# Kernel optimization log

Measured on AMD Instinct MI355X. Metric: run time of the kernel, lower is better.

The kernel has to match this reference:

```python
import jax, jax.numpy as jnp
import numpy as np

NH = 4       # n_heads
R = 3        # n_rounds
LN_EPS = 1e-5
NEG = -1e9   # large negative for masked attention (avoids NaN on fully-masked rows)


def _mha(q, k, v, w, b, block=None):
    # w: [4, D, D] = (Wq, Wk, Wv, Wo); b: [4, D]. batch_first MHA, no dropout (eval).
    B, Nq, Dm = q.shape
    hd = Dm // NH

    def proj(x, wi, bi):
        return (x @ wi + bi).reshape(B, -1, NH, hd).transpose(0, 2, 1, 3)  # [B,h,N,hd]

    Q = proj(q, w[0], b[0])
    K = proj(k, w[1], b[1])
    V = proj(v, w[2], b[2])
    s = jnp.einsum('bhqd,bhkd->bhqk', Q, K) * (1.0 / np.sqrt(hd))
    if block is not None:  # block[b,q,k]=True means masked out
        s = jnp.where(block[:, None, :, :], NEG, s)
    p = jax.nn.softmax(s, axis=-1)
    o = jnp.einsum('bhqk,bhkd->bhqd', p, V).transpose(0, 2, 1, 3).reshape(B, -1, Dm)
    return o @ w[3] + b[3]


def setup_inputs() -> dict:
    key = jax.random.key(0)
    ks = jax.random.split(key, 16)
    B, N, Dm = 256, 128, 256
    s = 0.02
    return {
        'H': jax.random.normal(ks[0], (B, N, Dm), jnp.float32),
        'pred_heads': jax.random.randint(ks[1], (B, N), 0, N),
        'mask': jnp.ones((B, N), jnp.float32),
        'ha_w': jax.random.normal(ks[2], (R, 4, Dm, Dm)) * s,
        'ha_b': jnp.zeros((R, 4, Dm)),
        'sa_w': jax.random.normal(ks[3], (R, 4, Dm, Dm)) * s,
        'sa_b': jnp.zeros((R, 4, Dm)),
        'ct_w': jax.random.normal(ks[4], (R, 2 * Dm, Dm)) * s,
        'ct_b': jnp.zeros((R, Dm)),
        'gate_w': jax.random.normal(ks[5], (R, 4 * Dm, Dm)) * s,
        'gate_b': jnp.zeros((R, Dm)),
        'tr_w': jax.random.normal(ks[6], (R, 4 * Dm, Dm)) * s,
        'tr_b': jnp.zeros((R, Dm)),
        'ln_g': jnp.ones((R, Dm)),
        'ln_b': jnp.zeros((R, Dm)),
        'arc_head_w': jax.random.normal(ks[7], (Dm, Dm)) * s,
        'arc_head_b': jnp.zeros((Dm,)),
        'arc_dep_w': jax.random.normal(ks[8], (Dm, Dm)) * s,
        'arc_dep_b': jnp.zeros((Dm,)),
        'bilinear': jax.random.normal(ks[9], (Dm, Dm)) * np.sqrt(2.0 / Dm).astype(np.float32),
        'bh_w': jax.random.normal(ks[10], (Dm,)) * s,
        'bh_b': jnp.zeros(()),
        'bd_w': jax.random.normal(ks[11], (Dm,)) * s,
        'bd_b': jnp.zeros(()),
    }


def reference(H, pred_heads, mask, ha_w, ha_b, sa_w, sa_b, ct_w, ct_b,
              gate_w, gate_b, tr_w, tr_b, ln_g, ln_b,
              arc_head_w, arc_head_b, arc_dep_w, arc_dep_b, bilinear,
              bh_w, bh_b, bd_w, bd_b):
    B, N, Dm = H.shape
    mb = mask > 0
    hi = jnp.clip(pred_heads, 0, N - 1)
    hi3 = jnp.broadcast_to(hi[:, :, None], (B, N, Dm))
    bidx = jnp.arange(B)[:, None]
    eye = jnp.eye(N, dtype=bool)
    # sibling mask: same predicted head, not self, both positions valid (constant across rounds)
    sib = (pred_heads[:, :, None] == pred_heads[:, None, :]) & ~eye[None] \
          & mb[:, None, :] & mb[:, :, None]
    block = ~sib

    Hr = H
    for i in range(R):
        # gather head representation, attend to it
        head_repr = jnp.take_along_axis(Hr, hi3, axis=1)
        head_msg = _mha(Hr, head_repr, head_repr, ha_w[i], ha_b[i])
        # scatter-add children onto their heads, average
        child_sum = jnp.zeros_like(Hr).at[bidx, hi].add(Hr)
        child_count = jnp.zeros((B, N), Hr.dtype).at[bidx, hi].add(mask)
        child_avg = child_sum / jnp.maximum(child_count, 1.0)[:, :, None]
        child_msg = jax.nn.gelu(
            jnp.concatenate([Hr, child_avg], -1) @ ct_w[i] + ct_b[i], approximate=False)
        # masked sibling self-attention (N <= 128 branch)
        sib_msg = _mha(Hr, Hr, Hr, sa_w[i], sa_b[i], block=block)
        # gated fuse + residual + LayerNorm
        comb = jnp.concatenate([Hr, head_msg, child_msg, sib_msg], -1)
        g = jax.nn.sigmoid(comb @ gate_w[i] + gate_b[i])
        u = jax.nn.gelu(comb @ tr_w[i] + tr_b[i], approximate=False)
        Hn = Hr + g * u
        mu = Hn.mean(-1, keepdims=True)
        var = ((Hn - mu) ** 2).mean(-1, keepdims=True)
        Hr = (Hn - mu) / jnp.sqrt(var + LN_EPS) * ln_g[i] + ln_b[i]

    h_head = Hr @ arc_head_w + arc_head_b
    h_dep = Hr @ arc_dep_w + arc_dep_b
    scores = jnp.einsum('bnd,de,bme->bnm', h_head, bilinear, h_dep)
    scores = scores + (h_head @ bh_w + bh_b)[:, None, :] + (h_dep @ bd_w + bd_b)[:, :, None]
    return Hr, scores
```

## Files before the change

### kernel.cpp

```cpp
#include <hip/hip_runtime.h>
#include <hip/hip_bf16.h>
#include <math.h>

typedef __hip_bfloat16 bf16;
typedef __attribute__((ext_vector_type(8))) short bf16x8v;
typedef __attribute__((ext_vector_type(4))) float f32x4v;

#define BD 256
#define NN 128
#define DM 256
#define NHD 4
#define HDIM 64
#define RR 3

__device__ __forceinline__ float b2f(bf16 x) { return __bfloat162float(x); }
__device__ __forceinline__ bf16 f2b(float x) { return __float2bfloat16(x); }
__device__ __forceinline__ float geluf(float x) { return 0.5f * x * (1.f + erff(x * 0.70710678118654752f)); }

#define GLOAD16(g, l) __builtin_amdgcn_global_load_lds( \
    (const __attribute__((address_space(1))) void*)(g), \
    (__attribute__((address_space(3))) void*)(l), 16, 0, 0)

__global__ __launch_bounds__(256) void cvt32to16_kernel(
    const float* __restrict__ in, bf16* __restrict__ out, int n)
{
  int i = blockIdx.x * 256 + threadIdx.x;
  int stride = gridDim.x * 256;
  for (; i < n; i += stride) out[i] = f2b(in[i]);
}

__global__ __launch_bounds__(256) void cvt16to32_kernel(
    const bf16* __restrict__ in, float* __restrict__ out, int n)
{
  int i = blockIdx.x * 256 + threadIdx.x;
  int stride = gridDim.x * 256;
  for (; i < n; i += stride) out[i] = b2f(in[i]);
}

struct TDesc { const float* src; bf16* dst; int K; int base; };
struct TTable { TDesc e[11]; };

__global__ __launch_bounds__(256) void transpose_w_kernel(TTable T, int nent)
{
  int t = blockIdx.x;
  int ei = 0;
  for (int i = 1; i < nent; i++) if (t >= T.e[i].base) ei = i;
  const float* src = T.e[ei].src;
  bf16* dst = T.e[ei].dst;
  int K = T.e[ei].K;
  int lt = t - T.e[ei].base;
  int nt = lt & 7, kt = lt >> 3;

  __shared__ float tile[32][33];
  int tx = threadIdx.x & 31, ty = threadIdx.x >> 5;
#pragma unroll
  for (int i = 0; i < 4; i++)
    tile[ty + i * 8][tx] = src[(size_t)(kt * 32 + ty + i * 8) * 256 + nt * 32 + tx];
  __syncthreads();
#pragma unroll
  for (int i = 0; i < 4; i++)
    dst[(size_t)(nt * 32 + ty + i * 8) * K + kt * 32 + tx] = f2b(tile[tx][ty + i * 8]);
}

struct GJob {
  const bf16 *a0, *a1, *a2, *a3;
  const int* gather;
  const bf16* Wt;
  const float* bias;
  bf16* out;
  int K, act, transp;
};
struct GJobs8 { GJob j[8]; };

__global__ __launch_bounds__(256) void gemm_multi_kernel(GJobs8 J)
{
  const GJob jb = J.j[blockIdx.y];
  const int b  = blockIdx.x & 255;
  const int nh = blockIdx.x >> 8;
  const int tid = threadIdx.x;
  const int w = tid >> 6;
  const int lane = tid & 63;
  const int wr = w >> 1, wc = w & 1;
  const int r16 = lane & 15;
  const int kg = lane >> 4;
  const int K = jb.K;
  const int nk = K >> 5;
  const int c0 = nh * 128;

  __shared__ __align__(16) char lds[32768];

  const int srow = tid >> 2;
  const int skc  = tid & 3;
  int g0 = srow, g1 = srow + 64;
  if (jb.gather) {
    int t0 = jb.gather[b * NN + srow];      g0 = min(max(t0, 0), NN - 1);
    int t1 = jb.gather[b * NN + srow + 64]; g1 = min(max(t1, 0), NN - 1);
  }
  const size_t aoff0 = ((size_t)b * NN + g0) * DM + skc * 8;
  const size_t aoff1 = ((size_t)b * NN + g1) * DM + skc * 8;
  const bf16* wsrc0 = jb.Wt + (size_t)(c0 + srow) * K + skc * 8;
  const bf16* wsrc1 = jb.Wt + (size_t)(c0 + srow + 64) * K + skc * 8;
  const int wbase = w * 1024;

  f32x4v zero = {0.f, 0.f, 0.f, 0.f};
  f32x4v acc[4][4];
#pragma unroll
  for (int mi = 0; mi < 4; mi++)
#pragma unroll
    for (int ni = 0; ni < 4; ni++) acc[mi][ni] = zero;

  int a_ro[4], w_ro[4];
#pragma unroll
  for (int mi = 0; mi < 4; mi++)
    a_ro[mi] = (wr * 64 + mi * 16 + r16) * 64 + kg * 16;
#pragma unroll
  for (int ni = 0; ni < 4; ni++)
    w_ro[ni] = (wc * 64 + ni * 16 + r16) * 64 + kg * 16;

  {
    const bf16* Ab = jb.a0;
    GLOAD16(Ab + aoff0, lds + wbase);
    GLOAD16(Ab + aoff1, lds + 4096 + wbase);
    GLOAD16(wsrc0,      lds + 16384 + wbase);
    GLOAD16(wsrc1,      lds + 16384 + 4096 + wbase);
  }
  __syncthreads();

  int cur = 0;
  for (int kt = 0; kt < nk; kt++) {
    if (kt + 1 < nk) {
      int k0 = (kt + 1) << 5;
      int sg = k0 >> 8;
      const bf16* Ab = (sg == 0) ? jb.a0 : ((sg == 1) ? jb.a1 : ((sg == 2) ? jb.a2 : jb.a3));
      int ko = k0 & 255;
      int nb = (cur ^ 1) * 8192;
      GLOAD16(Ab + aoff0 + ko,  lds + nb + wbase);
      GLOAD16(Ab + aoff1 + ko,  lds + nb + 4096 + wbase);
      GLOAD16(wsrc0 + k0,       lds + 16384 + nb + wbase);
      GLOAD16(wsrc1 + k0,       lds + 16384 + nb + 4096 + wbase);
    }

    const char* La = lds + cur * 8192;
    const char* Lw = lds + 16384 + cur * 8192;
    bf16x8v a[4], ww[4];
#pragma unroll
    for (int mi = 0; mi < 4; mi++) a[mi] = *(const bf16x8v*)(La + a_ro[mi]);
#pragma unroll
    for (int ni = 0; ni < 4; ni++) ww[ni] = *(const bf16x8v*)(Lw + w_ro[ni]);
#pragma unroll
    for (int mi = 0; mi < 4; mi++)
#pragma unroll
      for (int ni = 0; ni < 4; ni++)
        acc[mi][ni] = __builtin_amdgcn_mfma_f32_16x16x32_bf16(a[mi], ww[ni], acc[mi][ni], 0, 0, 0);

    __syncthreads();
    cur ^= 1;
  }

#pragma unroll
  for (int ni = 0; ni < 4; ni++) {
    int col = c0 + wc * 64 + ni * 16 + r16;
    float bv = jb.bias ? jb.bias[col] : 0.f;
#pragma unroll
    for (int mi = 0; mi < 4; mi++) {
      int row0 = wr * 64 + mi * 16 + kg * 4;
      if (!jb.transp) {
        size_t base = ((size_t)b * NN + row0) * DM + col;
#pragma unroll
        for (int r = 0; r < 4; r++) {
          float x = acc[mi][ni][r] + bv;
          if (jb.act == 1) x = geluf(x);
          jb.out[base + (size_t)r * DM] = f2b(x);
        }
      } else {
        size_t base = ((size_t)b * DM + col) * NN + row0;
#pragma unroll
        for (int r = 0; r < 4; r++) {
          float x = acc[mi][ni][r] + bv;
          if (jb.act == 1) x = geluf(x);
          jb.out[base + r] = f2b(x);
        }
      }
    }
  }
}

struct AttnArgs {
  const bf16 *Qa, *Ka, *Va; bf16* Oa;
  const bf16 *Qs, *Ks, *Vs; bf16* Os;
};

__global__ __launch_bounds__(256) void attn2_kernel(
    AttnArgs A, const int* __restrict__ ph, const float* __restrict__ mask)
{
  const int b = blockIdx.y, h = blockIdx.x;
  const bool has_mask = (blockIdx.z == 1);
  const bf16* Qb = has_mask ? A.Qs : A.Qa;
  const bf16* Kb = has_mask ? A.Ks : A.Ka;
  const bf16* Vt = has_mask ? A.Vs : A.Va;
  bf16* Ob       = has_mask ? A.Os : A.Oa;

  const int w = threadIdx.x >> 6;
  const int lane = threadIdx.x & 63;
  const int r16 = lane & 15, kg = lane >> 4;
  const int q0 = w * 32;

  __shared__ bf16 P_lds[4][32 * 128];
  __shared__ int   ph_sh[NN];
  __shared__ float mk_sh[NN];

  if (has_mask && threadIdx.x < NN) {
    ph_sh[threadIdx.x] = ph[(size_t)b * NN + threadIdx.x];
    mk_sh[threadIdx.x] = mask[(size_t)b * NN + threadIdx.x];
  }
  __syncthreads();

  const bf16* Qh = Qb + (size_t)b * NN * DM + (size_t)h * HDIM;
  const bf16* Kh = Kb + (size_t)b * NN * DM + (size_t)h * HDIM;
  const bf16* Vh = Vt + ((size_t)b * DM + (size_t)h * HDIM) * NN;

  f32x4v zero = {0.f, 0.f, 0.f, 0.f};

  f32x4v accs[2][8];
#pragma unroll
  for (int mi = 0; mi < 2; mi++)
#pragma unroll
    for (int ni = 0; ni < 8; ni++) accs[mi][ni] = zero;

#pragma unroll
  for (int ks = 0; ks < 2; ks++) {
    int d = ks * 32 + kg * 8;
    bf16x8v a[2], bb[8];
#pragma unroll
    for (int mi = 0; mi < 2; mi++)
      a[mi] = *(const bf16x8v*)(Qh + (size_t)(q0 + mi * 16 + r16) * DM + d);
#pragma unroll
    for (int ni = 0; ni < 8; ni++)
      bb[ni] = *(const bf16x8v*)(Kh + (size_t)(ni * 16 + r16) * DM + d);
#pragma unroll
    for (int mi = 0; mi < 2; mi++)
#pragma unroll
      for (int ni = 0; ni < 8; ni++)
        accs[mi][ni] = __builtin_amdgcn_mfma_f32_16x16x32_bf16(a[mi], bb[ni], accs[mi][ni], 0, 0, 0);
  }

#pragma unroll
  for (int mi = 0; mi < 2; mi++) {
#pragma unroll
    for (int r = 0; r < 4; r++) {
      int wq = mi * 16 + kg * 4 + r;
      int q_e = q0 + wq;
      float v[8];
      float mx = -3.0e38f;
      int qp = 0; float qm = 1.f;
      if (has_mask) { qp = ph_sh[q_e]; qm = mk_sh[q_e]; }
#pragma unroll
      for (int ni = 0; ni < 8; ni++) {
        float s = accs[mi][ni][r] * 0.125f;
        if (has_mask) {
          int t_e = ni * 16 + r16;
          bool sib = (qp == ph_sh[t_e]) && (q_e != t_e) && (qm > 0.f) && (mk_sh[t_e] > 0.f);
          if (!sib) s = -1e9f;
        }
        v[ni] = s;
        mx = fmaxf(mx, s);
      }
#pragma unroll
      for (int o = 1; o < 16; o <<= 1) mx = fmaxf(mx, __shfl_xor(mx, o, 64));
      float sum = 0.f;
#pragma unroll
      for (int ni = 0; ni < 8; ni++) { v[ni] = __expf(v[ni] - mx); sum += v[ni]; }
#pragma unroll
      for (int o = 1; o < 16; o <<= 1) sum += __shfl_xor(sum, o, 64);
      float inv = 1.f / sum;
      int swz = (wq & 7) << 3;
#pragma unroll
      for (int ni = 0; ni < 8; ni++) {
        int t_e = ni * 16 + r16;
        P_lds[w][(wq * 128 + t_e) ^ swz] = f2b(v[ni] * inv);
      }
    }
  }
  __syncthreads();

  f32x4v acco[2][4];
#pragma unroll
  for (int mi = 0; mi < 2; mi++)
#pragma unroll
    for (int ni = 0; ni < 4; ni++) acco[mi][ni] = zero;

#pragma unroll
  for (int kt = 0; kt < 4; kt++) {
    int t = kt * 32 + kg * 8;
    bf16x8v a[2], bb[4];
#pragma unroll
    for (int mi = 0; mi < 2; mi++) {
      int wqr = mi * 16 + r16;
      int idx = (wqr * 128 + t) ^ ((wqr & 7) << 3);
      a[mi] = *(const bf16x8v*)&P_lds[w][idx];
    }
#pragma unroll
    for (int ni = 0; ni < 4; ni++)
      bb[ni] = *(const bf16x8v*)(Vh + (size_t)(ni * 16 + r16) * NN + t);
#pragma unroll
    for (int mi = 0; mi < 2; mi++)
#pragma unroll
      for (int ni = 0; ni < 4; ni++)
        acco[mi][ni] = __builtin_amdgcn_mfma_f32_16x16x32_bf16(a[mi], bb[ni], acco[mi][ni], 0, 0, 0);
  }

#pragma unroll
  for (int ni = 0; ni < 4; ni++) {
    int d = ni * 16 + r16;
#pragma unroll
    for (int mi = 0; mi < 2; mi++) {
      int qrow = q0 + mi * 16 + kg * 4;
      size_t base = ((size_t)b * NN + qrow) * DM + (size_t)h * HDIM + d;
#pragma unroll
      for (int r = 0; r < 4; r++)
        Ob[base + (size_t)r * DM] = f2b(acco[mi][ni][r]);
    }
  }
}

__global__ __launch_bounds__(256) void child_avg2_kernel(
    const bf16* __restrict__ Hr, const int* __restrict__ ph,
    const float* __restrict__ mask, bf16* __restrict__ CA)
{
  const int b = blockIdx.x;
  const int t = threadIdx.x;
  __shared__ int hi[NN];
  __shared__ float mk[NN];
  __shared__ int cnt[NN], off[NN], rnk[NN], lst[NN];
  __shared__ float cntf[NN];

  if (t < NN) {
    int g = ph[(size_t)b * NN + t];
    hi[t] = min(max(g, 0), NN - 1);
    mk[t] = mask[(size_t)b * NN + t];
  }
  __syncthreads();
  if (t < NN) {
    int c = 0, r = 0; float cf = 0.f;
    int me = hi[t];
    for (int j = 0; j < NN; j++) {
      int hj = hi[j];
      c  += (hj == t);
      cf += (hj == t) ? mk[j] : 0.f;
      r  += (j < t) && (hj == me);
    }
    cnt[t] = c; cntf[t] = cf; rnk[t] = r;
  }
  __syncthreads();
  if (t < NN) {
    int o = 0;
    for (int m = 0; m < t; m++) o += cnt[m];
    off[t] = o;
  }
  __syncthreads();
  if (t < NN) lst[off[hi[t]] + rnk[t]] = t;
  __syncthreads();

  const bf16* Hb = Hr + (size_t)b * NN * DM;
  bf16* Cb = CA + (size_t)b * NN * DM;
  const int d = t;
  for (int m = 0; m < NN; m++) {
    float s = 0.f;
    int o = off[m], c = cnt[m];
    for (int i = 0; i < c; i++)
      s += b2f(Hb[(size_t)lst[o + i] * DM + d]);
    Cb[(size_t)m * DM + d] = f2b(s / fmaxf(cntf[m], 1.f));
  }
}

__global__ __launch_bounds__(256) void ln_epi_kernel(
    const bf16* __restrict__ Hr, const bf16* __restrict__ Gp, const bf16* __restrict__ Up,
    const float* __restrict__ lg, const float* __restrict__ lb, bf16* __restrict__ Hout)
{
  const int b = blockIdx.y;
  const int m0 = blockIdx.x * 8;
  const int c = threadIdx.x;
  __shared__ float red[8];
  float lgv = lg[c], lbv = lb[c];
  int wv = c >> 6, ln = c & 63;
  for (int m = 0; m < 8; m++) {
    size_t idx = ((size_t)b * NN + m0 + m) * DM + c;
    float g = 1.f / (1.f + __expf(-b2f(Gp[idx])));
    float u = geluf(b2f(Up[idx]));
    float hn = b2f(Hr[idx]) + g * u;
    float s1 = hn, s2 = hn * hn;
#pragma unroll
    for (int o = 1; o < 64; o <<= 1) { s1 += __shfl_xor(s1, o, 64); s2 += __shfl_xor(s2, o, 64); }
    if (ln == 0) { red[wv] = s1; red[4 + wv] = s2; }
    __syncthreads();
    float sum = red[0] + red[1] + red[2] + red[3];
    float sq  = red[4] + red[5] + red[6] + red[7];
    float mu = sum * (1.f / DM);
    float var = sq * (1.f / DM) - mu * mu;
    float y = (hn - mu) * rsqrtf(var + 1e-5f) * lgv + lbv;
    Hout[idx] = f2b(y);
    __syncthreads();
  }
}

__global__ __launch_bounds__(256) void rhrd_kernel(
    const bf16* __restrict__ hh, const bf16* __restrict__ hd,
    const float* __restrict__ bhw, const float* __restrict__ bhb,
    const float* __restrict__ bdw, const float* __restrict__ bdb,
    float* __restrict__ rh, float* __restrict__ rd)
{
  int b = blockIdx.x;
  int t = threadIdx.x;
  int n = t & 127;
  bool isD = t >= 128;
  const bf16* row = (isD ? hd : hh) + ((size_t)b * NN + n) * DM;
  const float* wv = isD ? bdw : bhw;
  float s = isD ? bdb[0] : bhb[0];
  for (int k = 0; k < DM; k++) s += b2f(row[k]) * wv[k];
  (isD ? rd : rh)[(size_t)b * NN + n] = s;
}

__global__ __launch_bounds__(512) void scores_mfma_kernel(
    const bf16* __restrict__ tmp, const bf16* __restrict__ hd,
    const float* __restrict__ rh, const float* __restrict__ rd,
    float* __restrict__ out)
{
  const int b = blockIdx.x;
  const int w = threadIdx.x >> 6;
  const int lane = threadIdx.x & 63;
  const int wr = w >> 1, wc = w & 1;
  const int r16 = lane & 15;
  const int kg = lane >> 4;

  size_t qoff[2], moff[4];
#pragma unroll
  for (int mi = 0; mi < 2; mi++) qoff[mi] = ((size_t)b * NN + wr * 32 + mi * 16 + r16) * DM;
#pragma unroll
  for (int ni = 0; ni < 4; ni++) moff[ni] = ((size_t)b * NN + wc * 64 + ni * 16 + r16) * DM;

  f32x4v zero = {0.f, 0.f, 0.f, 0.f};
  f32x4v acc[2][4];
#pragma unroll
  for (int mi = 0; mi < 2; mi++)
#pragma unroll
    for (int ni = 0; ni < 4; ni++) acc[mi][ni] = zero;

  for (int k0 = 0; k0 < DM; k0 += 32) {
    int k = k0 + kg * 8;
    bf16x8v a[2], bb[4];
#pragma unroll
    for (int mi = 0; mi < 2; mi++) a[mi] = *(const bf16x8v*)(tmp + qoff[mi] + k);
#pragma unroll
    for (int ni = 0; ni < 4; ni++) bb[ni] = *(const bf16x8v*)(hd + moff[ni] + k);
#pragma unroll
    for (int mi = 0; mi < 2; mi++)
#pragma unroll
      for (int ni = 0; ni < 4; ni++)
        acc[mi][ni] = __builtin_amdgcn_mfma_f32_16x16x32_bf16(a[mi], bb[ni], acc[mi][ni], 0, 0, 0);
  }

#pragma unroll
  for (int ni = 0; ni < 4; ni++) {
    int m = wc * 64 + ni * 16 + r16;
    float rhm = rh[b * NN + m];
#pragma unroll
    for (int mi = 0; mi < 2; mi++) {
      int q0 = wr * 32 + mi * 16 + kg * 4;
#pragma unroll
      for (int r = 0; r < 4; r++)
        out[(size_t)b * NN * NN + (size_t)(q0 + r) * NN + m] =
            acc[mi][ni][r] + rhm + rd[b * NN + q0 + r];
    }
  }
}

extern "C" void kernel_launch(void* const* d_in, const int* in_sizes, int n_in,
                              void* d_out, int out_size, void* d_ws, size_t ws_size,
                              hipStream_t stream) {
  const float* H      = (const float*)d_in[0];
  const int*   ph     = (const int*)  d_in[1];
  const float* mask   = (const float*)d_in[2];
  const float* ha_w   = (const float*)d_in[3];
  const float* ha_b   = (const float*)d_in[4];
  const float* sa_w   = (const float*)d_in[5];
  const float* sa_b   = (const float*)d_in[6];
  const float* ct_w   = (const float*)d_in[7];
  const float* ct_b   = (const float*)d_in[8];
  const float* gate_w = (const float*)d_in[9];
  const float* gate_b = (const float*)d_in[10];
  const float* tr_w   = (const float*)d_in[11];
  const float* tr_b   = (const float*)d_in[12];
  const float* ln_g   = (const float*)d_in[13];
  const float* ln_b   = (const float*)d_in[14];
  const float* ahw    = (const float*)d_in[15];
  const float* ahb    = (const float*)d_in[16];
  const float* adw    = (const float*)d_in[17];
  const float* adb    = (const float*)d_in[18];
  const float* bil    = (const float*)d_in[19];
  const float* bhw    = (const float*)d_in[20];
  const float* bhb    = (const float*)d_in[21];
  const float* bdw    = (const float*)d_in[22];
  const float* bdb    = (const float*)d_in[23];

  const size_t AB = (size_t)BD * NN * DM;
  bf16* wsb  = (bf16*)d_ws;
  bf16* Hcur = wsb + 0 * AB;
  bf16* Qa   = wsb + 1 * AB;
  bf16* Ka   = wsb + 2 * AB;
  bf16* Va   = wsb + 3 * AB;
  bf16* Qs   = wsb + 4 * AB;
  bf16* Ks   = wsb + 5 * AB;
  bf16* Vs   = wsb + 6 * AB;
  bf16* mC   = wsb + 7 * AB;
  float* rh  = (float*)(wsb + 8 * AB);
  float* rd  = rh + (size_t)BD * NN;

  bf16* D0 = (bf16*)d_out;
  bf16* D1 = D0 + AB;
  bf16* D2 = D0 + 2 * AB;
  bf16* haT = D2;
  bf16* saT = D2 + 262144;
  bf16* ctT = D2 + 524288;
  bf16* gT  = D2 + 655360;
  bf16* tT  = D2 + 917504;

  cvt32to16_kernel<<<dim3(2048), 256, 0, stream>>>(H, Hcur, (int)AB);

  for (int r = 0; r < RR; r++) {
    TTable T; int base = 0;
    for (int i = 0; i < 4; i++) {
      T.e[i] = { ha_w + ((size_t)r * 4 + i) * 65536, haT + (size_t)i * 65536, 256, base };
      base += 64;
    }
    for (int i = 0; i < 4; i++) {
      T.e[4 + i] = { sa_w + ((size_t)r * 4 + i) * 65536, saT + (size_t)i * 65536, 256, base };
      base += 64;
    }
    T.e[8]  = { ct_w   + (size_t)r * 131072, ctT, 512,  base }; base += 128;
    T.e[9]  = { gate_w + (size_t)r * 262144, gT,  1024, base }; base += 256;
    T.e[10] = { tr_w   + (size_t)r * 262144, tT,  1024, base }; base += 256;
    transpose_w_kernel<<<dim3(base), 256, 0, stream>>>(T, 11);

    child_avg2_kernel<<<dim3(BD), 256, 0, stream>>>(Hcur, ph, mask, D0);

    const float* hab = ha_b + (size_t)r * 4 * DM;
    const float* sab = sa_b + (size_t)r * 4 * DM;

    {
      GJobs8 J = {};
      J.j[0] = { Hcur, Hcur, Hcur, Hcur, nullptr, haT,          hab + 0,   Qa, 256, 0, 0 };
      J.j[1] = { Hcur, Hcur, Hcur, Hcur, ph,      haT + 65536,  hab + 256, Ka, 256, 0, 0 };
      J.j[2] = { Hcur, Hcur, Hcur, Hcur, ph,      haT + 131072, hab + 512, Va, 256, 0, 1 };
      J.j[3] = { Hcur, Hcur, Hcur, Hcur, nullptr, saT,          sab + 0,   Qs, 256, 0, 0 };
      J.j[4] = { Hcur, Hcur, Hcur, Hcur, nullptr, saT + 65536,  sab + 256, Ks, 256, 0, 0 };
      J.j[5] = { Hcur, Hcur, Hcur, Hcur, nullptr, saT + 131072, sab + 512, Vs, 256, 0, 1 };
      J.j[6] = { Hcur, D0,   Hcur, Hcur, nullptr, ctT, ct_b + (size_t)r * DM, mC, 512, 1, 0 };
      gemm_multi_kernel<<<dim3(512, 7), 256, 0, stream>>>(J);
    }

    {
      AttnArgs A = { Qa, Ka, Va, D0, Qs, Ks, Vs, D1 };
      attn2_kernel<<<dim3(NHD, BD, 2), 256, 0, stream>>>(A, ph, mask);
    }

    {
      GJobs8 J = {};
      J.j[0] = { D0, D0, D0, D0, nullptr, haT + 196608, hab + 768, Ka, 256, 0, 0 };
      J.j[1] = { D1, D1, D1, D1, nullptr, saT + 196608, sab + 768, Ks, 256, 0, 0 };
      gemm_multi_kernel<<<dim3(512, 2), 256, 0, stream>>>(J);
    }

    {
      GJobs8 J = {};
      J.j[0] = { Hcur, Ka, mC, Ks, nullptr, gT, gate_b + (size_t)r * DM, Va, 1024, 0, 0 };
      J.j[1] = { Hcur, Ka, mC, Ks, nullptr, tT, tr_b   + (size_t)r * DM, Vs, 1024, 0, 0 };
      gemm_multi_kernel<<<dim3(512, 2), 256, 0, stream>>>(J);
    }

    ln_epi_kernel<<<dim3(16, BD), 256, 0, stream>>>(Hcur, Va, Vs,
        ln_g + (size_t)r * DM, ln_b + (size_t)r * DM, Hcur);
  }

  {
    TTable T;
    T.e[0] = { ahw, D2,           256, 0 };
    T.e[1] = { adw, D2 + 65536,   256, 64 };
    T.e[2] = { bil, D2 + 131072,  256, 128 };
    transpose_w_kernel<<<dim3(192), 256, 0, stream>>>(T, 3);
  }
  {
    GJobs8 J = {};
    J.j[0] = { Hcur, Hcur, Hcur, Hcur, nullptr, D2,          ahb, Qa, 256, 0, 0 };
    J.j[1] = { Hcur, Hcur, Hcur, Hcur, nullptr, D2 + 65536,  adb, Ka, 256, 0, 0 };
    gemm_multi_kernel<<<dim3(512, 2), 256, 0, stream>>>(J);
  }
  rhrd_kernel<<<dim3(BD), 256, 0, stream>>>(Qa, Ka, bhw, bhb, bdw, bdb, rh, rd);
  {
    GJobs8 J = {};
    J.j[0] = { Qa, Qa, Qa, Qa, nullptr, D2 + 131072, nullptr, Va, 256, 0, 0 };
    gemm_multi_kernel<<<dim3(512, 1), 256, 0, stream>>>(J);
  }
  scores_mfma_kernel<<<dim3(BD), 512, 0, stream>>>(Va, Ka, rh, rd, (float*)d_out + AB);

  cvt16to32_kernel<<<dim3(2048), 256, 0, stream>>>(Hcur, (float*)d_out, (int)AB);
}
```

Baseline: 1.042 ms.

## Fuse seven projection GEMMs into one kernel reusing LDS-resident H tile

Replaces the seven-job projection launch with a single kernel per (batch, column-half) block. The block loads the 128x256 H tile into LDS once and reuses it for all seven weight projections, including the gathered rows for the head-attention K and V. Weight tiles are double-buffered and prefetched across job boundaries. It also adds an XOR swizzle to the LDS layout of the generic GEMM to avoid bank conflicts. The trade-offs are 80KB of LDS per block, which lowers occupancy, and a launch of only 512 blocks, so less parallelism. The child-average operand is read directly from global memory without staging.

```diff
diff --git a/kernel.cpp b/kernel.cpp
--- a/kernel.cpp
+++ b/kernel.cpp
@@ -60,6 +60,147 @@
 #pragma unroll
   for (int i = 0; i < 4; i++)
     dst[(size_t)(nt * 32 + ty + i * 8) * K + kt * 32 + tx] = f2b(tile[tx][ty + i * 8]);
+}
+
+struct ProjArgs {
+  const bf16* Hc; const bf16* CA; const int* gather;
+  const bf16* W[7];
+  const float* bias[7];
+  bf16* out[7];
+};
+
+__global__ __launch_bounds__(256) void proj_fused_kernel(ProjArgs P)
+{
+  const int b  = blockIdx.x & 255;
+  const int nh = blockIdx.x >> 8;
+  const int c0 = nh * 128;
+  const int tid = threadIdx.x;
+  const int w = tid >> 6;
+  const int lane = tid & 63;
+  const int wr = w >> 1, wc = w & 1;
+  const int r16 = lane & 15;
+  const int kg = lane >> 4;
+
+  __shared__ __align__(16) char lds[81920];
+
+  const char* Hb = (const char*)(P.Hc + (size_t)b * NN * DM);
+
+#pragma unroll
+  for (int i = 0; i < 16; i++) {
+    int row = w * 32 + i * 2 + (lane >> 5);
+    int src = row * 512 + (((lane & 31) * 16) ^ ((row & 7) << 4));
+    GLOAD16(Hb + src, lds + w * 16384 + i * 1024);
+  }
+
+#define STAGE_W(WT, K2, KT, BUF) do { \
+    _Pragma("unroll") \
+    for (int i_ = 0; i_ < 2; i_++) { \
+      int wrow_ = w * 32 + i_ * 16 + (lane >> 2); \
+      int slot_ = (lane & 3) ^ ((wrow_ >> 1) & 3); \
+      GLOAD16((const char*)(WT) + (size_t)(c0 + wrow_) * (K2) + (KT) * 64 + slot_ * 16, \
+              lds + 65536 + (BUF) * 8192 + w * 2048 + i_ * 1024); \
+    } } while (0)
+
+  STAGE_W(P.W[0], 512, 0, 0);
+  __syncthreads();
+
+  int lrow[4], grow[4];
+#pragma unroll
+  for (int mi = 0; mi < 4; mi++) {
+    lrow[mi] = wr * 64 + mi * 16 + r16;
+    int g = P.gather[b * NN + lrow[mi]];
+    grow[mi] = min(max(g, 0), NN - 1);
+  }
+  int wro[4];
+#pragma unroll
+  for (int ni = 0; ni < 4; ni++) {
+    int ct_ = wc * 64 + ni * 16 + r16;
+    wro[ni] = ct_ * 64 + ((kg ^ ((ct_ >> 1) & 3)) << 4);
+  }
+
+  const bf16* CAb = P.CA + (size_t)b * NN * DM;
+  int buf = 0;
+  f32x4v zero = {0.f, 0.f, 0.f, 0.f};
+
+#pragma unroll
+  for (int j = 0; j < 7; j++) {
+    const bool GATH = (j == 1) || (j == 2);
+    const bool TR   = (j == 2) || (j == 5);
+    const bool ACT  = (j == 6);
+    const int NKS = (j == 6) ? 16 : 8;
+    const int K2  = (j == 6) ? 1024 : 512;
+    const bf16* Wj  = P.W[j];
+    const bf16* Wj1 = (j < 6) ? P.W[j + 1] : P.W[j];
+    const int  K2n  = (j < 6) ? ((j + 1 == 6) ? 1024 : 512) : K2;
+
+    f32x4v acc[4][4];
+#pragma unroll
+    for (int mi = 0; mi < 4; mi++)
+#pragma unroll
+      for (int ni = 0; ni < 4; ni++) acc[mi][ni] = zero;
+
+    for (int kt = 0; kt < NKS; kt++) {
+      if (!(j == 6 && kt + 1 == NKS)) {
+        const bf16* Wn = (kt + 1 < NKS) ? Wj : Wj1;
+        int nkt = (kt + 1 < NKS) ? kt + 1 : 0;
+        int nK2 = (kt + 1 < NKS) ? K2 : K2n;
+        STAGE_W(Wn, nK2, nkt, buf ^ 1);
+      }
+
+      bf16x8v a[4], wv[4];
+      if (j == 6 && kt >= 8) {
+#pragma unroll
+        for (int mi = 0; mi < 4; mi++)
+          a[mi] = *(const bf16x8v*)(CAb + (size_t)lrow[mi] * DM + (kt - 8) * 32 + kg * 8);
+      } else {
+#pragma unroll
+        for (int mi = 0; mi < 4; mi++) {
+          int ar = GATH ? grow[mi] : lrow[mi];
+          int off = ar * 512 + (((kt * 64) + kg * 16) ^ ((ar & 7) << 4));
+          a[mi] = *(const bf16x8v*)(lds + off);
+        }
+      }
+#pragma unroll
+      for (int ni = 0; ni < 4; ni++)
+        wv[ni] = *(const bf16x8v*)(lds + 65536 + buf * 8192 + wro[ni]);
+
+#pragma unroll
+      for (int mi = 0; mi < 4; mi++)
+#pragma unroll
+        for (int ni = 0; ni < 4; ni++)
+          acc[mi][ni] = __builtin_amdgcn_mfma_f32_16x16x32_bf16(a[mi], wv[ni], acc[mi][ni], 0, 0, 0);
+
+      __syncthreads();
+      buf ^= 1;
+    }
+
+    bf16* outj = P.out[j];
+    const float* bj = P.bias[j];
+#pragma unroll
+    for (int ni = 0; ni < 4; ni++) {
+      int col = c0 + wc * 64 + ni * 16 + r16;
+      float bv = bj ? bj[col] : 0.f;
+#pragma unroll
+      for (int mi = 0; mi < 4; mi++) {
+        int row0 = wr * 64 + mi * 16 + kg * 4;
+        if (!TR) {
+          size_t base = ((size_t)b * NN + row0) * DM + col;
+#pragma unroll
+          for (int r = 0; r < 4; r++) {
+            float x = acc[mi][ni][r] + bv;
+            if (ACT) x = geluf(x);
+            outj[base + (size_t)r * DM] = f2b(x);
+          }
+        } else {
+          size_t base = ((size_t)b * DM + col) * NN + row0;
+#pragma unroll
+          for (int r = 0; r < 4; r++)
+            outj[base + r] = f2b(acc[mi][ni][r] + bv);
+        }
+      }
+    }
+  }
+#undef STAGE_W
 }
 
 struct GJob {
@@ -91,15 +232,16 @@
 
   const int srow = tid >> 2;
   const int skc  = tid & 3;
+  const int sl   = skc ^ ((srow >> 1) & 3);
   int g0 = srow, g1 = srow + 64;
   if (jb.gather) {
     int t0 = jb.gather[b * NN + srow];      g0 = min(max(t0, 0), NN - 1);
     int t1 = jb.gather[b * NN + srow + 64]; g1 = min(max(t1, 0), NN - 1);
   }
-  const size_t aoff0 = ((size_t)b * NN + g0) * DM + skc * 8;
-  const size_t aoff1 = ((size_t)b * NN + g1) * DM + skc * 8;
-  const bf16* wsrc0 = jb.Wt + (size_t)(c0 + srow) * K + skc * 8;
-  const bf16* wsrc1 = jb.Wt + (size_t)(c0 + srow + 64) * K + skc * 8;
+  const size_t aoff0 = ((size_t)b * NN + g0) * DM + sl * 8;
+  const size_t aoff1 = ((size_t)b * NN + g1) * DM + sl * 8;
+  const bf16* wsrc0 = jb.Wt + (size_t)(c0 + srow) * K + sl * 8;
+  const bf16* wsrc1 = jb.Wt + (size_t)(c0 + srow + 64) * K + sl * 8;
   const int wbase = w * 1024;
 
   f32x4v zero = {0.f, 0.f, 0.f, 0.f};
@@ -111,11 +253,15 @@
 
   int a_ro[4], w_ro[4];
 #pragma unroll
-  for (int mi = 0; mi < 4; mi++)
-    a_ro[mi] = (wr * 64 + mi * 16 + r16) * 64 + kg * 16;
-#pragma unroll
-  for (int ni = 0; ni < 4; ni++)
-    w_ro[ni] = (wc * 64 + ni * 16 + r16) * 64 + kg * 16;
+  for (int mi = 0; mi < 4; mi++) {
+    int row = wr * 64 + mi * 16 + r16;
+    a_ro[mi] = row * 64 + ((kg ^ ((row >> 1) & 3)) << 4);
+  }
+#pragma unroll
+  for (int ni = 0; ni < 4; ni++) {
+    int col = wc * 64 + ni * 16 + r16;
+    w_ro[ni] = col * 64 + ((kg ^ ((col >> 1) & 3)) << 4);
+  }
 
   {
     const bf16* Ab = jb.a0;
@@ -547,15 +693,16 @@
     const float* sab = sa_b + (size_t)r * 4 * DM;
 
     {
-      GJobs8 J = {};
-      J.j[0] = { Hcur, Hcur, Hcur, Hcur, nullptr, haT,          hab + 0,   Qa, 256, 0, 0 };
-      J.j[1] = { Hcur, Hcur, Hcur, Hcur, ph,      haT + 65536,  hab + 256, Ka, 256, 0, 0 };
-      J.j[2] = { Hcur, Hcur, Hcur, Hcur, ph,      haT + 131072, hab + 512, Va, 256, 0, 1 };
-      J.j[3] = { Hcur, Hcur, Hcur, Hcur, nullptr, saT,          sab + 0,   Qs, 256, 0, 0 };
-      J.j[4] = { Hcur, Hcur, Hcur, Hcur, nullptr, saT + 65536,  sab + 256, Ks, 256, 0, 0 };
-      J.j[5] = { Hcur, Hcur, Hcur, Hcur, nullptr, saT + 131072, sab + 512, Vs, 256, 0, 1 };
-      J.j[6] = { Hcur, D0,   Hcur, Hcur, nullptr, ctT, ct_b + (size_t)r * DM, mC, 512, 1, 0 };
-      gemm_multi_kernel<<<dim3(512, 7), 256, 0, stream>>>(J);
+      ProjArgs P;
+      P.Hc = Hcur; P.CA = D0; P.gather = ph;
+      P.W[0] = haT;          P.bias[0] = hab + 0;   P.out[0] = Qa;
+      P.W[1] = haT + 65536;  P.bias[1] = hab + 256; P.out[1] = Ka;
+      P.W[2] = haT + 131072; P.bias[2] = hab + 512; P.out[2] = Va;
+      P.W[3] = saT;          P.bias[3] = sab + 0;   P.out[3] = Qs;
+      P.W[4] = saT + 65536;  P.bias[4] = sab + 256; P.out[4] = Ks;
+      P.W[5] = saT + 131072; P.bias[5] = sab + 512; P.out[5] = Vs;
+      P.W[6] = ctT;          P.bias[6] = ct_b + (size_t)r * DM; P.out[6] = mC;
+      proj_fused_kernel<<<dim3(512), 256, 0, stream>>>(P);
     }
 
     {
```

Measured after the change: 1.027 ms. About the same (-1.5%).
